# Kernel tuning notes

Measured on AMD Instinct MI355X. Metric: run time of the kernel, lower is better.

## Reference

```python
import jax, jax.numpy as jnp
import numpy as np

B, N, D, C, IN, S = 64, 8192, 64, 256, 128, 3
CTRL_IN = IN + D  # input concatenated with 1 read vector
EPS = 1e-8


def _address(h, mem, prev_w, Wk, bk, Wb, bb, Wg, bg, Ws, bs, Wgam, bgam):
    """NTM content+location addressing. h:[B,C], mem:[B,N,D], prev_w:[B,N] -> [B,N]."""
    k = h @ Wk + bk                                   # [B,D]
    beta = jax.nn.softplus(h @ Wb + bb)               # [B,1]
    g = jax.nn.sigmoid(h @ Wg + bg)                   # [B,1]
    s = jax.nn.softmax(h @ Ws + bs, axis=-1)          # [B,S]
    gamma = jax.nn.softplus(h @ Wgam + bgam) + 1.0    # [B,1]
    # cosine similarity of key vs each memory row
    dots = jnp.einsum('bnd,bd->bn', mem, k)           # [B,N]
    norms = jnp.linalg.norm(mem, axis=-1) * jnp.linalg.norm(k, axis=-1, keepdims=True)
    sim = dots / (norms + EPS)
    wc = jax.nn.softmax(beta * sim, axis=-1)          # content weights
    wg = g * wc + (1.0 - g) * prev_w                  # interpolation gate
    # circular convolution with shift kernel, offsets [-1, 0, 1]
    offsets = [j - S // 2 for j in range(S)]
    ws = sum(s[:, j:j + 1] * jnp.roll(wg, offsets[j], axis=1) for j in range(S))
    # sharpening
    wpow = ws ** gamma
    return wpow / (jnp.sum(wpow, axis=-1, keepdims=True) + EPS)


def setup_inputs() -> dict:
    key = jax.random.key(0)
    ks = jax.random.split(key, 40)

    def p(k, shape):
        return jax.random.normal(k, shape, jnp.float32) / np.sqrt(shape[0]).astype(np.float32)

    inp = {
        'x': jax.random.normal(ks[0], (B, IN), jnp.float32),
        'prev_memory': jax.random.uniform(ks[1], (B, N, D), jnp.float32),
        'prev_read_weights': jax.random.uniform(ks[2], (B, N), jnp.float32),
        'prev_write_weights': jax.random.uniform(ks[3], (B, N), jnp.float32),
        'prev_read_vector': jax.random.normal(ks[4], (B, D), jnp.float32),
        # feedforward controller
        'W_ctrl': p(ks[5], (CTRL_IN, C)), 'b_ctrl': jnp.zeros((C,), jnp.float32),
        # read head
        'Wk_r': p(ks[6], (C, D)), 'bk_r': jnp.zeros((D,), jnp.float32),
        'Wb_r': p(ks[7], (C, 1)), 'bb_r': jnp.zeros((1,), jnp.float32),
        'Wg_r': p(ks[8], (C, 1)), 'bg_r': jnp.zeros((1,), jnp.float32),
        'Ws_r': p(ks[9], (C, S)), 'bs_r': jnp.zeros((S,), jnp.float32),
        'Wgam_r': p(ks[10], (C, 1)), 'bgam_r': jnp.zeros((1,), jnp.float32),
        # write head
        'Wk_w': p(ks[11], (C, D)), 'bk_w': jnp.zeros((D,), jnp.float32),
        'Wb_w': p(ks[12], (C, 1)), 'bb_w': jnp.zeros((1,), jnp.float32),
        'Wg_w': p(ks[13], (C, 1)), 'bg_w': jnp.zeros((1,), jnp.float32),
        'Ws_w': p(ks[14], (C, S)), 'bs_w': jnp.zeros((S,), jnp.float32),
        'Wgam_w': p(ks[15], (C, 1)), 'bgam_w': jnp.zeros((1,), jnp.float32),
        'We_w': p(ks[16], (C, D)), 'be_w': jnp.zeros((D,), jnp.float32),
        'Wa_w': p(ks[17], (C, D)), 'ba_w': jnp.zeros((D,), jnp.float32),
    }
    return inp


def reference(x, prev_memory, prev_read_weights, prev_write_weights, prev_read_vector,
              W_ctrl, b_ctrl,
              Wk_r, bk_r, Wb_r, bb_r, Wg_r, bg_r, Ws_r, bs_r, Wgam_r, bgam_r,
              Wk_w, bk_w, Wb_w, bb_w, Wg_w, bg_w, Ws_w, bs_w, Wgam_w, bgam_w,
              We_w, be_w, Wa_w, ba_w):
    # controller: Dense + relu over [input, prev read vector]
    ctrl_in = jnp.concatenate([x, prev_read_vector], axis=-1)    # [B, CTRL_IN]
    h = jax.nn.relu(ctrl_in @ W_ctrl + b_ctrl)                   # [B, C]

    # write head: addressing, then erase/add memory update
    w_w = _address(h, prev_memory, prev_write_weights,
                   Wk_w, bk_w, Wb_w, bb_w, Wg_w, bg_w, Ws_w, bs_w, Wgam_w, bgam_w)
    erase = jax.nn.sigmoid(h @ We_w + be_w)                      # [B, D]
    add = jnp.tanh(h @ Wa_w + ba_w)                              # [B, D]
    ww = w_w[:, :, None]                                         # [B, N, 1]
    new_memory = prev_memory * (1.0 - ww * erase[:, None, :]) + ww * add[:, None, :]

    # read head: addressing on updated memory, then weighted read
    w_r = _address(h, new_memory, prev_read_weights,
                   Wk_r, bk_r, Wb_r, bb_r, Wg_r, bg_r, Ws_r, bs_r, Wgam_r, bgam_r)
    read_vec = jnp.einsum('bnd,bn->bd', new_memory, w_r)         # [B, D]

    output = jnp.concatenate([h, read_vec], axis=-1)             # [B, C + D]
    return output
```

## Files before the change

kernel.cpp:

```cpp
#include <hip/hip_runtime.h>
#include <math.h>

#define Bb   64
#define Nn   8192
#define Dd   64
#define Cc   256
#define INn  128
#define CTRL 192
#define OUTW 320
#define EPSF 1e-8f
#define BN   (Bb*Nn)

#define OFF_P4  0
#define OFF_P2  (4*BN)
#define OFF_WPW (6*BN)
#define OFF_WPR (7*BN)
#define OFF_PT  (8*BN)
#define OFF_MS  (OFF_PT + 2048*64)
#define OFF_PW  (OFF_MS + 4096)
#define OFF_MSR (OFF_PW + 2048)
#define OFF_PR  (OFF_MSR + 4096)
#define OFF_KW  (OFF_PR + 2048)
#define OFF_KR  (OFF_KW + Bb*Dd)
#define OFF_ER  (OFF_KR + Bb*Dd)
#define OFF_AD  (OFF_ER + Bb*Dd)
#define OFF_SC  (OFF_AD + Bb*Dd)

__device__ __forceinline__ float softplusf(float x) {
    return (x > 20.f) ? x : log1pf(__expf(x));
}
__device__ __forceinline__ float sigmoidf(float x) {
    return 1.f / (1.f + __expf(-x));
}
__device__ __forceinline__ void msCombine(float& m, float& s, float m2, float s2) {
    const float mn = fmaxf(m, m2);
    s = s * __expf(m - mn) + s2 * __expf(m2 - mn);
    m = mn;
}

struct SetupArgs {
    const float *x, *prv, *Wc, *bc;
    const float *Wk_r, *bk_r, *Wb_r, *bb_r, *Wg_r, *bg_r, *Ws_r, *bs_r, *Wgam_r, *bgam_r;
    const float *Wk_w, *bk_w, *Wb_w, *bb_w, *Wg_w, *bg_w, *Ws_w, *bs_w, *Wgam_w, *bgam_w;
    const float *We_w, *be_w, *Wa_w, *ba_w;
    float *ws, *out;
};

__global__ __launch_bounds__(256) void k_setup(SetupArgs a) {
    __shared__ float ci[CTRL];
    __shared__ float h[Cc];
    __shared__ alignas(16) float kbuf[128];
    __shared__ alignas(16) float abuf[64];
    __shared__ float red[4][16];
    __shared__ float sums[16];
    const int b = blockIdx.x, t = threadIdx.x;

    if (t < INn)       ci[t] = a.x[b * INn + t];
    else if (t < CTRL) ci[t] = a.prv[b * Dd + (t - INn)];
    __syncthreads();

    float acc = a.bc[t];
    #pragma unroll 16
    for (int i = 0; i < CTRL; ++i) acc += ci[i] * a.Wc[i * Cc + t];
    const float hv = fmaxf(acc, 0.f);
    h[t] = hv;
    a.out[b * OUTW + t] = hv;
    __syncthreads();

    {
        const int job = t >> 6, d = t & 63;
        const float* W  = (job == 0) ? a.Wk_w : (job == 1) ? a.Wk_r : (job == 2) ? a.We_w : a.Wa_w;
        const float* bs = (job == 0) ? a.bk_w : (job == 1) ? a.bk_r : (job == 2) ? a.be_w : a.ba_w;
        float p = bs[d];
        #pragma unroll 16
        for (int c = 0; c < Cc; ++c) p += h[c] * W[c * Dd + d];
        if (job == 0)      { a.ws[OFF_KW + b * Dd + d] = p; kbuf[d] = p; }
        else if (job == 1) { a.ws[OFF_KR + b * Dd + d] = p; kbuf[64 + d] = p; }
        else if (job == 2) { a.ws[OFF_ER + b * Dd + d] = sigmoidf(p); }
        else               { const float ad = tanhf(p); a.ws[OFF_AD + b * Dd + d] = ad; abuf[d] = ad; }
    }
    __syncthreads();

    float v[16];
    v[0] = hv * a.Wb_w[t];  v[1] = hv * a.Wg_w[t];  v[2] = hv * a.Wgam_w[t];
    v[3] = hv * a.Ws_w[t * 3 + 0]; v[4] = hv * a.Ws_w[t * 3 + 1]; v[5] = hv * a.Ws_w[t * 3 + 2];
    v[6] = hv * a.Wb_r[t];  v[7] = hv * a.Wg_r[t];  v[8] = hv * a.Wgam_r[t];
    v[9] = hv * a.Ws_r[t * 3 + 0]; v[10] = hv * a.Ws_r[t * 3 + 1]; v[11] = hv * a.Ws_r[t * 3 + 2];
    v[12] = (t < 64) ? kbuf[t] * kbuf[t] : 0.f;
    v[13] = (t >= 64 && t < 128) ? kbuf[t] * kbuf[t] : 0.f;
    v[14] = (t < 64) ? abuf[t] * kbuf[64 + t] : 0.f;
    v[15] = (t < 64) ? abuf[t] * abuf[t] : 0.f;
    #pragma unroll
    for (int k = 0; k < 16; ++k) {
        #pragma unroll
        for (int m = 32; m >= 1; m >>= 1) v[k] += __shfl_xor(v[k], m);
    }
    if ((t & 63) == 0) {
        #pragma unroll
        for (int k = 0; k < 16; ++k) red[t >> 6][k] = v[k];
    }
    __syncthreads();
    if (t < 16) sums[t] = red[0][t] + red[1][t] + red[2][t] + red[3][t];
    __syncthreads();

    if (t == 0) {
        float* sc = a.ws + OFF_SC + b * 16;
        sc[0] = softplusf(sums[0] + a.bb_w[0]);
        sc[1] = sigmoidf(sums[1] + a.bg_w[0]);
        sc[2] = softplusf(sums[2] + a.bgam_w[0]) + 1.f;
        sc[3] = sqrtf(sums[12]);
        sc[4] = softplusf(sums[6] + a.bb_r[0]);
        sc[5] = sigmoidf(sums[7] + a.bg_r[0]);
        sc[6] = softplusf(sums[8] + a.bgam_r[0]) + 1.f;
        sc[7] = sqrtf(sums[13]);
        {
            const float v0 = sums[3] + a.bs_w[0], v1 = sums[4] + a.bs_w[1], v2 = sums[5] + a.bs_w[2];
            const float m = fmaxf(fmaxf(v0, v1), v2);
            const float e0 = __expf(v0 - m), e1 = __expf(v1 - m), e2 = __expf(v2 - m);
            const float s = e0 + e1 + e2;
            sc[8] = e0 / s; sc[9] = e1 / s; sc[10] = e2 / s;
        }
        sc[11] = sums[14];
        {
            const float v0 = sums[9] + a.bs_r[0], v1 = sums[10] + a.bs_r[1], v2 = sums[11] + a.bs_r[2];
            const float m = fmaxf(fmaxf(v0, v1), v2);
            const float e0 = __expf(v0 - m), e1 = __expf(v1 - m), e2 = __expf(v2 - m);
            const float s = e0 + e1 + e2;
            sc[12] = e0 / s; sc[13] = e1 / s; sc[14] = e2 / s;
        }
        sc[15] = sums[15];
    }
}

__global__ __launch_bounds__(256) void k_pass1(const float* __restrict__ mem,
                                               float* __restrict__ ws) {
    __shared__ float tr[4][64 * 49];
    __shared__ float wm[4], wsum[4];
    const int t = threadIdx.x;
    const int wv = t >> 6, lane = t & 63;
    const int cg = lane & 7;
    const int rr = lane >> 3;
    const int tile = (blockIdx.x << 2) + wv;
    const int rowbase = tile << 6;
    const int b = rowbase >> 13;
    const int cb = cg << 3;

    const float4 kwA = *(const float4*)(ws + OFF_KW + (b << 6) + cb);
    const float4 kwB = *(const float4*)(ws + OFF_KW + (b << 6) + cb + 4);
    const float4 krA = *(const float4*)(ws + OFF_KR + (b << 6) + cb);
    const float4 krB = *(const float4*)(ws + OFF_KR + (b << 6) + cb + 4);
    const float4 evA = *(const float4*)(ws + OFF_ER + (b << 6) + cb);
    const float4 evB = *(const float4*)(ws + OFF_ER + (b << 6) + cb + 4);
    const float4 avA = *(const float4*)(ws + OFF_AD + (b << 6) + cb);
    const float4 avB = *(const float4*)(ws + OFF_AD + (b << 6) + cb + 4);
    const float beta = ws[OFF_SC + b * 16 + 0];
    const float kn   = ws[OFF_SC + b * 16 + 3];

    float acc[8][6];
    #pragma unroll
    for (int s = 0; s < 8; ++s) {
        const int row = rowbase + (s << 3) + rr;
        const float* mp = mem + ((size_t)row << 6) + cb;
        const float4 m0 = *(const float4*)(mp);
        const float4 m1 = *(const float4*)(mp + 4);
        float dw = 0.f, dr = 0.f, nq = 0.f, e1 = 0.f, e2 = 0.f, c5 = 0.f;
        #define ACC(mv, kwv, krv, evv, avv) { \
            const float me = (mv) * (evv); \
            dw = fmaf((mv), (kwv), dw); \
            dr = fmaf((mv), (krv), dr); \
            nq = fmaf((mv), (mv), nq); \
            e1 = fmaf((mv), (avv) - me, e1); \
            e2 = fmaf(me, fmaf(-2.f, (avv), me), e2); \
            c5 = fmaf(me, (krv), c5); }
        ACC(m0.x, kwA.x, krA.x, evA.x, avA.x)
        ACC(m0.y, kwA.y, krA.y, evA.y, avA.y)
        ACC(m0.z, kwA.z, krA.z, evA.z, avA.z)
        ACC(m0.w, kwA.w, krA.w, evA.w, avA.w)
        ACC(m1.x, kwB.x, krB.x, evB.x, avB.x)
        ACC(m1.y, kwB.y, krB.y, evB.y, avB.y)
        ACC(m1.z, kwB.z, krB.z, evB.z, avB.z)
        ACC(m1.w, kwB.w, krB.w, evB.w, avB.w)
        #undef ACC
        acc[s][0] = dw; acc[s][1] = dr; acc[s][2] = nq;
        acc[s][3] = e1; acc[s][4] = e2; acc[s][5] = c5;
    }

    float* T = tr[wv];
    #pragma unroll
    for (int s = 0; s < 8; ++s) {
        #pragma unroll
        for (int v = 0; v < 6; ++v)
            T[((s << 3) + rr) * 49 + cg * 6 + v] = acc[s][v];
    }
    __syncthreads();

    float dw = 0.f, dr = 0.f, nq = 0.f, e1 = 0.f, e2 = 0.f, c5 = 0.f;
    #pragma unroll
    for (int g = 0; g < 8; ++g) {
        const float* p = T + lane * 49 + g * 6;
        dw += p[0]; dr += p[1]; nq += p[2];
        e1 += p[3]; e2 += p[4]; c5 += p[5];
    }
    const int row = rowbase + lane;
    const float xw = beta * dw / (sqrtf(nq) * kn + EPSF);
    {
        float4 p4; p4.x = xw; p4.y = dr; p4.z = c5; p4.w = nq;
        *(float4*)(ws + OFF_P4 + ((size_t)row << 2)) = p4;
        float2 p2; p2.x = e1; p2.y = e2;
        *(float2*)(ws + OFF_P2 + ((size_t)row << 1)) = p2;
    }

    float om = xw, os = 1.f;
    #pragma unroll
    for (int mk = 1; mk <= 32; mk <<= 1) {
        const float m2 = __shfl_xor(om, mk), s2 = __shfl_xor(os, mk);
        msCombine(om, os, m2, s2);
    }
    if (lane == 0) { wm[wv] = om; wsum[wv] = os; }
    __syncthreads();
    if (t == 0) {
        float M = wm[0], S = wsum[0];
        msCombine(M, S, wm[1], wsum[1]);
        msCombine(M, S, wm[2], wsum[2]);
        msCombine(M, S, wm[3], wsum[3]);
        ws[OFF_MS + (blockIdx.x << 1)]     = M;
        ws[OFF_MS + (blockIdx.x << 1) + 1] = S;
    }
}

__global__ __launch_bounds__(256) void k_wside(const float* __restrict__ prevw_w,
                                               float* __restrict__ ws) {
    __shared__ float wgbuf[258];
    __shared__ float red[6];
    const int blk = blockIdx.x, t = threadIdx.x;
    const int b = blk >> 5;
    const int rbl = (blk & 31) << 8;
    const int bN = b * Nn;

    if (t < 64) {
        float m = -1e30f, s = 0.f;
        if (t < 32) {
            m = ws[OFF_MS + (((b << 5) + t) << 1)];
            s = ws[OFF_MS + (((b << 5) + t) << 1) + 1];
        }
        #pragma unroll
        for (int mk = 1; mk <= 32; mk <<= 1) {
            const float m2 = __shfl_xor(m, mk), s2 = __shfl_xor(s, mk);
            msCombine(m, s, m2, s2);
        }
        if (t == 0) { red[4] = m; red[5] = 1.f / s; }
    }
    __syncthreads();
    const float M = red[4], invS = red[5];
    const float* sc = ws + OFF_SC + b * 16;
    const float g = sc[1], gam = sc[2];
    const float s0 = sc[8], s1 = sc[9], s2 = sc[10];

    auto wg_at = [&](int i) {
        const int rg = bN + ((rbl + i - 1) & (Nn - 1));
        const float xw = ws[OFF_P4 + ((size_t)rg << 2)];
        return g * __expf(xw - M) * invS + (1.f - g) * prevw_w[rg];
    };
    wgbuf[t + 1] = wg_at(t + 1);
    if (t == 0)   wgbuf[0]   = wg_at(0);
    if (t == 255) wgbuf[257] = wg_at(257);
    __syncthreads();

    const float wsv = s0 * wgbuf[t + 2] + s1 * wgbuf[t + 1] + s2 * wgbuf[t];
    const float wp = __expf(gam * __logf(wsv));
    ws[OFF_WPW + bN + rbl + t] = wp;

    float v = wp;
    #pragma unroll
    for (int mk = 1; mk <= 32; mk <<= 1) v += __shfl_xor(v, mk);
    if ((t & 63) == 0) red[t >> 6] = v;
    __syncthreads();
    if (t == 0) ws[OFF_PW + blk] = red[0] + red[1] + red[2] + red[3];
}

__global__ __launch_bounds__(256) void k_rside(float* __restrict__ ws) {
    __shared__ float redm[4], reds[4];
    __shared__ float inv[1];
    const int blk = blockIdx.x, t = threadIdx.x;
    const int b = blk >> 5;
    const int rbl = (blk & 31) << 8;
    const int bN = b * Nn;

    if (t < 64) {
        float v = (t < 32) ? ws[OFF_PW + (b << 5) + t] : 0.f;
        #pragma unroll
        for (int mk = 1; mk <= 32; mk <<= 1) v += __shfl_xor(v, mk);
        if (t == 0) inv[0] = 1.f / (v + EPSF);
    }
    __syncthreads();
    const float invW = inv[0];
    const float* sc = ws + OFF_SC + b * 16;
    const float beta_r = sc[4], kn_r = sc[7], AK = sc[11], A2 = sc[15];

    const int row = bN + rbl + t;
    const float ww = ws[OFF_WPW + row] * invW;
    const float4 p4 = *(const float4*)(ws + OFF_P4 + ((size_t)row << 2));
    const float2 p2 = *(const float2*)(ws + OFF_P2 + ((size_t)row << 1));
    const float d = p4.y + ww * (AK - p4.z);
    float qq = p4.w + 2.f * ww * p2.x + ww * ww * (p2.y + A2);
    qq = fmaxf(qq, 0.f);
    const float x = beta_r * d / (sqrtf(qq) * kn_r + EPSF);
    ws[OFF_P2 + ((size_t)row << 1)] = x;

    float om = x, os = 1.f;
    #pragma unroll
    for (int mk = 1; mk <= 32; mk <<= 1) {
        const float m2 = __shfl_xor(om, mk), s2 = __shfl_xor(os, mk);
        msCombine(om, os, m2, s2);
    }
    if ((t & 63) == 0) { redm[t >> 6] = om; reds[t >> 6] = os; }
    __syncthreads();
    if (t == 0) {
        float M = redm[0], S = reds[0];
        msCombine(M, S, redm[1], reds[1]);
        msCombine(M, S, redm[2], reds[2]);
        msCombine(M, S, redm[3], reds[3]);
        ws[OFF_MSR + (blk << 1)]     = M;
        ws[OFF_MSR + (blk << 1) + 1] = S;
    }
}

__global__ __launch_bounds__(256) void k_rfin(const float* __restrict__ prevw_r,
                                              float* __restrict__ ws) {
    __shared__ float wgbuf[258];
    __shared__ float red[6];
    const int blk = blockIdx.x, t = threadIdx.x;
    const int b = blk >> 5;
    const int rbl = (blk & 31) << 8;
    const int bN = b * Nn;

    if (t < 64) {
        float m = -1e30f, s = 0.f;
        if (t < 32) {
            m = ws[OFF_MSR + (((b << 5) + t) << 1)];
            s = ws[OFF_MSR + (((b << 5) + t) << 1) + 1];
        }
        #pragma unroll
        for (int mk = 1; mk <= 32; mk <<= 1) {
            const float m2 = __shfl_xor(m, mk), s2 = __shfl_xor(s, mk);
            msCombine(m, s, m2, s2);
        }
        if (t == 0) { red[4] = m; red[5] = 1.f / s; }
    }
    __syncthreads();
    const float M = red[4], invS = red[5];
    const float* sc = ws + OFF_SC + b * 16;
    const float g = sc[5], gam = sc[6];
    const float s0 = sc[12], s1 = sc[13], s2 = sc[14];

    auto wg_at = [&](int i) {
        const int rg = bN + ((rbl + i - 1) & (Nn - 1));
        const float xr = ws[OFF_P2 + ((size_t)rg << 1)];
        return g * __expf(xr - M) * invS + (1.f - g) * prevw_r[rg];
    };
    wgbuf[t + 1] = wg_at(t + 1);
    if (t == 0)   wgbuf[0]   = wg_at(0);
    if (t == 255) wgbuf[257] = wg_at(257);
    __syncthreads();

    const float wsv = s0 * wgbuf[t + 2] + s1 * wgbuf[t + 1] + s2 * wgbuf[t];
    const float wp = __expf(gam * __logf(wsv));
    ws[OFF_WPR + bN + rbl + t] = wp;

    float v = wp;
    #pragma unroll
    for (int mk = 1; mk <= 32; mk <<= 1) v += __shfl_xor(v, mk);
    if ((t & 63) == 0) red[t >> 6] = v;
    __syncthreads();
    if (t == 0) ws[OFF_PR + blk] = red[0] + red[1] + red[2] + red[3];
}

__global__ __launch_bounds__(256) void k_read(const float* __restrict__ mem,
                                              float* __restrict__ ws) {
    __shared__ float lds[4 * 64];
    __shared__ float invb[2];
    const int b = blockIdx.x >> 5;
    const int chunk = blockIdx.x & 31;
    const int t = threadIdx.x;
    const int lane = t & 63, wv = t >> 6;
    const int q = lane & 15, r = lane >> 4;

    if (t < 64) {
        float vw = (t < 32) ? ws[OFF_PW + (b << 5) + t] : 0.f;
        float vr = (t < 32) ? ws[OFF_PR + (b << 5) + t] : 0.f;
        #pragma unroll
        for (int mk = 1; mk <= 32; mk <<= 1) { vw += __shfl_xor(vw, mk); vr += __shfl_xor(vr, mk); }
        if (t == 0) { invb[0] = 1.f / (vw + EPSF); invb[1] = 1.f / (vr + EPSF); }
    }
    __syncthreads();
    const float invW = invb[0], invR = invb[1];

    const float4 evv = *(const float4*)(ws + OFF_ER + (b << 6) + (q << 2));
    const float4 avv = *(const float4*)(ws + OFF_AD + (b << 6) + (q << 2));
    float a0 = 0.f, a1 = 0.f, a2 = 0.f, a3 = 0.f;
    const int base_n = chunk << 8;
    #pragma unroll 4
    for (int gi = wv; gi < 64; gi += 4) {
        const int n = base_n + (gi << 2) + r;
        const int row = b * Nn + n;
        const float4 mv = *(const float4*)(mem + ((size_t)row << 6) + (q << 2));
        const float w   = ws[OFF_WPW + row] * invW;
        const float wrv = ws[OFF_WPR + row] * invR;
        a0 = fmaf((mv.x * (1.f - w * evv.x) + w * avv.x), wrv, a0);
        a1 = fmaf((mv.y * (1.f - w * evv.y) + w * avv.y), wrv, a1);
        a2 = fmaf((mv.z * (1.f - w * evv.z) + w * avv.z), wrv, a2);
        a3 = fmaf((mv.w * (1.f - w * evv.w) + w * avv.w), wrv, a3);
    }
    #pragma unroll
    for (int m = 16; m <= 32; m <<= 1) {
        a0 += __shfl_xor(a0, m); a1 += __shfl_xor(a1, m);
        a2 += __shfl_xor(a2, m); a3 += __shfl_xor(a3, m);
    }
    if (r == 0) {
        lds[wv * 64 + q * 4 + 0] = a0; lds[wv * 64 + q * 4 + 1] = a1;
        lds[wv * 64 + q * 4 + 2] = a2; lds[wv * 64 + q * 4 + 3] = a3;
    }
    __syncthreads();
    if (t < 64) {
        ws[OFF_PT + blockIdx.x * 64 + t] = lds[t] + lds[64 + t] + lds[128 + t] + lds[192 + t];
    }
}

__global__ __launch_bounds__(64) void k_reduce(const float* __restrict__ ws,
                                               float* __restrict__ out) {
    const int b = blockIdx.x, d = threadIdx.x;
    float s = 0.f;
    #pragma unroll
    for (int i = 0; i < 32; ++i) s += ws[OFF_PT + ((b << 5) + i) * 64 + d];
    out[b * OUTW + 256 + d] = s;
}

extern "C" void kernel_launch(void* const* d_in, const int* in_sizes, int n_in,
                              void* d_out, int out_size, void* d_ws, size_t ws_size,
                              hipStream_t stream) {
    const float* x      = (const float*)d_in[0];
    const float* mem    = (const float*)d_in[1];
    const float* prw_r  = (const float*)d_in[2];
    const float* prw_w  = (const float*)d_in[3];
    const float* prv    = (const float*)d_in[4];

    float* ws  = (float*)d_ws;
    float* out = (float*)d_out;

    SetupArgs a;
    a.x = x; a.prv = prv;
    a.Wc = (const float*)d_in[5];  a.bc = (const float*)d_in[6];
    a.Wk_r = (const float*)d_in[7];  a.bk_r = (const float*)d_in[8];
    a.Wb_r = (const float*)d_in[9];  a.bb_r = (const float*)d_in[10];
    a.Wg_r = (const float*)d_in[11]; a.bg_r = (const float*)d_in[12];
    a.Ws_r = (const float*)d_in[13]; a.bs_r = (const float*)d_in[14];
    a.Wgam_r = (const float*)d_in[15]; a.bgam_r = (const float*)d_in[16];
    a.Wk_w = (const float*)d_in[17]; a.bk_w = (const float*)d_in[18];
    a.Wb_w = (const float*)d_in[19]; a.bb_w = (const float*)d_in[20];
    a.Wg_w = (const float*)d_in[21]; a.bg_w = (const float*)d_in[22];
    a.Ws_w = (const float*)d_in[23]; a.bs_w = (const float*)d_in[24];
    a.Wgam_w = (const float*)d_in[25]; a.bgam_w = (const float*)d_in[26];
    a.We_w = (const float*)d_in[27]; a.be_w = (const float*)d_in[28];
    a.Wa_w = (const float*)d_in[29]; a.ba_w = (const float*)d_in[30];
    a.ws = ws; a.out = out;

    k_setup <<<Bb,   256, 0, stream>>>(a);
    k_pass1 <<<2048, 256, 0, stream>>>(mem, ws);
    k_wside <<<2048, 256, 0, stream>>>(prw_w, ws);
    k_rside <<<2048, 256, 0, stream>>>(ws);
    k_rfin  <<<2048, 256, 0, stream>>>(prw_r, ws);
    k_read  <<<2048, 256, 0, stream>>>(mem, ws);
    k_reduce<<<Bb,   64,  0, stream>>>(ws, out);
}
```

Baseline: 83.13 us.

## Halve pass1 tile rows, double grid, and split per-row workspace into separate arrays

The first pass over memory now has each wave handle 32 rows instead of 64, with a half-wave shuffle combining the column-group partials, and launches twice as many blocks. The per-row workspace is reorganised so the write score and the read score sit in their own contiguous arrays. The later kernels that gather scores with halo accesses now read them unit-stride instead of strided out of float4/float2 records. The per-block softmax partials double in count, and half the lanes sit idle during the store phase.

```diff
diff --git a/kernel.cpp b/kernel.cpp
--- a/kernel.cpp
+++ b/kernel.cpp
@@ -11,13 +11,15 @@
 #define EPSF 1e-8f
 #define BN   (Bb*Nn)
 
-#define OFF_P4  0
-#define OFF_P2  (4*BN)
-#define OFF_WPW (6*BN)
-#define OFF_WPR (7*BN)
-#define OFF_PT  (8*BN)
-#define OFF_MS  (OFF_PT + 2048*64)
-#define OFF_PW  (OFF_MS + 4096)
+#define OFF_XW  0
+#define OFF_P4  BN
+#define OFF_E2  (5*BN)
+#define OFF_XR  (6*BN)
+#define OFF_WPW (7*BN)
+#define OFF_WPR (8*BN)
+#define OFF_PT  (9*BN)
+#define OFF_MS  (OFF_PT + 131072)
+#define OFF_PW  (OFF_MS + 8192)
 #define OFF_MSR (OFF_PW + 2048)
 #define OFF_PR  (OFF_MSR + 4096)
 #define OFF_KW  (OFF_PR + 2048)
@@ -134,14 +136,14 @@
 
 __global__ __launch_bounds__(256) void k_pass1(const float* __restrict__ mem,
                                                float* __restrict__ ws) {
-    __shared__ float tr[4][64 * 49];
+    __shared__ float tr[4][32 * 49];
     __shared__ float wm[4], wsum[4];
     const int t = threadIdx.x;
     const int wv = t >> 6, lane = t & 63;
     const int cg = lane & 7;
     const int rr = lane >> 3;
     const int tile = (blockIdx.x << 2) + wv;
-    const int rowbase = tile << 6;
+    const int rowbase = tile << 5;
     const int b = rowbase >> 13;
     const int cb = cg << 3;
 
@@ -156,9 +158,9 @@
     const float beta = ws[OFF_SC + b * 16 + 0];
     const float kn   = ws[OFF_SC + b * 16 + 3];
 
-    float acc[8][6];
-    #pragma unroll
-    for (int s = 0; s < 8; ++s) {
+    float acc[4][6];
+    #pragma unroll
+    for (int s = 0; s < 4; ++s) {
         const int row = rowbase + (s << 3) + rr;
         const float* mp = mem + ((size_t)row << 6) + cb;
         const float4 m0 = *(const float4*)(mp);
@@ -187,27 +189,32 @@
 
     float* T = tr[wv];
     #pragma unroll
-    for (int s = 0; s < 8; ++s) {
+    for (int s = 0; s < 4; ++s) {
         #pragma unroll
         for (int v = 0; v < 6; ++v)
             T[((s << 3) + rr) * 49 + cg * 6 + v] = acc[s][v];
     }
     __syncthreads();
 
+    const int rd = lane & 31;
+    const int gb = (lane >> 5) << 2;
     float dw = 0.f, dr = 0.f, nq = 0.f, e1 = 0.f, e2 = 0.f, c5 = 0.f;
     #pragma unroll
-    for (int g = 0; g < 8; ++g) {
-        const float* p = T + lane * 49 + g * 6;
+    for (int g = 0; g < 4; ++g) {
+        const float* p = T + rd * 49 + (gb + g) * 6;
         dw += p[0]; dr += p[1]; nq += p[2];
         e1 += p[3]; e2 += p[4]; c5 += p[5];
     }
-    const int row = rowbase + lane;
+    dw += __shfl_xor(dw, 32); dr += __shfl_xor(dr, 32); nq += __shfl_xor(nq, 32);
+    e1 += __shfl_xor(e1, 32); e2 += __shfl_xor(e2, 32); c5 += __shfl_xor(c5, 32);
+
+    const int row = rowbase + rd;
     const float xw = beta * dw / (sqrtf(nq) * kn + EPSF);
-    {
-        float4 p4; p4.x = xw; p4.y = dr; p4.z = c5; p4.w = nq;
+    if (lane < 32) {
+        ws[OFF_XW + row] = xw;
+        float4 p4; p4.x = dr; p4.y = c5; p4.z = nq; p4.w = e1;
         *(float4*)(ws + OFF_P4 + ((size_t)row << 2)) = p4;
-        float2 p2; p2.x = e1; p2.y = e2;
-        *(float2*)(ws + OFF_P2 + ((size_t)row << 1)) = p2;
+        ws[OFF_E2 + row] = e2;
     }
 
     float om = xw, os = 1.f;
@@ -224,7 +231,7 @@
         msCombine(M, S, wm[2], wsum[2]);
         msCombine(M, S, wm[3], wsum[3]);
         ws[OFF_MS + (blockIdx.x << 1)]     = M;
-        ws[OFF_MS + (blockIdx.x << 1) + 1] = S;
+        ws[OFF_MS + (blockIdx.x << 1) + 1] = S * 0.5f;
     }
 }
 
@@ -238,11 +245,8 @@
     const int bN = b * Nn;
 
     if (t < 64) {
-        float m = -1e30f, s = 0.f;
-        if (t < 32) {
-            m = ws[OFF_MS + (((b << 5) + t) << 1)];
-            s = ws[OFF_MS + (((b << 5) + t) << 1) + 1];
-        }
+        float m = ws[OFF_MS + ((b * 64 + t) << 1)];
+        float s = ws[OFF_MS + ((b * 64 + t) << 1) + 1];
         #pragma unroll
         for (int mk = 1; mk <= 32; mk <<= 1) {
             const float m2 = __shfl_xor(m, mk), s2 = __shfl_xor(s, mk);
@@ -258,8 +262,7 @@
 
     auto wg_at = [&](int i) {
         const int rg = bN + ((rbl + i - 1) & (Nn - 1));
-        const float xw = ws[OFF_P4 + ((size_t)rg << 2)];
-        return g * __expf(xw - M) * invS + (1.f - g) * prevw_w[rg];
+        return g * __expf(ws[OFF_XW + rg] - M) * invS + (1.f - g) * prevw_w[rg];
     };
     wgbuf[t + 1] = wg_at(t + 1);
     if (t == 0)   wgbuf[0]   = wg_at(0);
@@ -300,12 +303,12 @@
     const int row = bN + rbl + t;
     const float ww = ws[OFF_WPW + row] * invW;
     const float4 p4 = *(const float4*)(ws + OFF_P4 + ((size_t)row << 2));
-    const float2 p2 = *(const float2*)(ws + OFF_P2 + ((size_t)row << 1));
-    const float d = p4.y + ww * (AK - p4.z);
-    float qq = p4.w + 2.f * ww * p2.x + ww * ww * (p2.y + A2);
+    const float e2 = ws[OFF_E2 + row];
+    const float d = p4.x + ww * (AK - p4.y);
+    float qq = p4.z + 2.f * ww * p4.w + ww * ww * (e2 + A2);
     qq = fmaxf(qq, 0.f);
     const float x = beta_r * d / (sqrtf(qq) * kn_r + EPSF);
-    ws[OFF_P2 + ((size_t)row << 1)] = x;
+    ws[OFF_XR + row] = x;
 
     float om = x, os = 1.f;
     #pragma unroll
@@ -355,8 +358,7 @@
 
     auto wg_at = [&](int i) {
         const int rg = bN + ((rbl + i - 1) & (Nn - 1));
-        const float xr = ws[OFF_P2 + ((size_t)rg << 1)];
-        return g * __expf(xr - M) * invS + (1.f - g) * prevw_r[rg];
+        return g * __expf(ws[OFF_XR + rg] - M) * invS + (1.f - g) * prevw_r[rg];
     };
     wgbuf[t + 1] = wg_at(t + 1);
     if (t == 0)   wgbuf[0]   = wg_at(0);
@@ -465,7 +467,7 @@
     a.ws = ws; a.out = out;
 
     k_setup <<<Bb,   256, 0, stream>>>(a);
-    k_pass1 <<<2048, 256, 0, stream>>>(mem, ws);
+    k_pass1 <<<4096, 256, 0, stream>>>(mem, ws);
     k_wside <<<2048, 256, 0, stream>>>(prw_w, ws);
     k_rside <<<2048, 256, 0, stream>>>(ws);
     k_rfin  <<<2048, 256, 0, stream>>>(prw_r, ws);
```

Result: no change. 83.11 us (-0.0%).
